# Performance work log

Measured on AMD Instinct MI355X. Metric: run time of the kernel, lower is better.

The kernel has to match this reference:

```python
import jax, jax.numpy as jnp
import numpy as np

START = 1  # strings_utils.SpecialSymbol.START
B, S, H, V = 16, 256, 512, 32000

def setup_inputs() -> dict:
    key = jax.random.key(0)
    ks = jax.random.split(key, 8)
    sc = 1.0 / np.sqrt(H)
    return {
        "target": jax.random.randint(ks[0], (B, S), 0, V, dtype=jnp.int64),
        "hidden_state": jax.random.normal(ks[1], (1, B, H), jnp.float32),
        "cell_state": jax.random.normal(ks[2], (1, B, H), jnp.float32),
        "embedding": jax.random.normal(ks[3], (V, H), jnp.float32) * 0.02,  # tied with out.weight
        "W_ih": jax.random.uniform(ks[4], (4 * H, H), jnp.float32, -sc, sc),
        "W_hh": jax.random.uniform(ks[5], (4 * H, H), jnp.float32, -sc, sc),
        "b_ih": jax.random.uniform(ks[6], (4 * H,), jnp.float32, -sc, sc),
        "b_hh": jax.random.uniform(ks[7], (4 * H,), jnp.float32, -sc, sc),
        "out_bias": jnp.zeros((V,), jnp.float32),
    }

def reference(target, hidden_state, cell_state, embedding, W_ih, W_hh, b_ih, b_hh, out_bias):
    # Teacher-forced decode: input at step 0 is START, then target[:, :-1]
    tokens = jnp.concatenate(
        [jnp.full((target.shape[0], 1), START, dtype=target.dtype), target[:, :-1]], axis=1
    )  # [B, S]
    emb = embedding[tokens]  # [B, S, H]
    # Precompute input contribution to gates for all steps (one big GEMM)
    xW = jnp.einsum("bsh,gh->bsg", emb, W_ih) + b_ih + b_hh  # [B, S, 4H]
    h0, c0 = hidden_state[0], cell_state[0]  # num_layers == 1

    def step(carry, x_t):
        h, c = carry
        gates = x_t + h @ W_hh.T  # [B, 4H]
        i, f, g, o = jnp.split(gates, 4, axis=-1)  # torch gate order: i, f, g, o
        i, f, o = jax.nn.sigmoid(i), jax.nn.sigmoid(f), jax.nn.sigmoid(o)
        g = jnp.tanh(g)
        c = f * c + i * g
        h = o * jnp.tanh(c)
        return (h, c), h

    (_, _), hs = jax.lax.scan(step, (h0, c0), jnp.swapaxes(xW, 0, 1))  # hs: [S, B, H]
    hs = jnp.swapaxes(hs, 0, 1)  # [B, S, H]
    logits = jnp.einsum("bsh,vh->bsv", hs, embedding) + out_bias  # tied projection [B, S, V]
    return logits
```

## Files before the change

kernel.cpp:

```cpp
#include <hip/hip_runtime.h>
#include <stdint.h>

#define B_N 16
#define S_N 256
#define H_N 512
#define V_N 32000
#define G4_N 2048
#define START_TOK 1
#define NBLK 16

typedef float f32x4 __attribute__((ext_vector_type(4)));
typedef int   i32x4 __attribute__((ext_vector_type(4)));
typedef unsigned short u16;
typedef u16 u16x4 __attribute__((ext_vector_type(4)));

static __device__ __forceinline__ u16 f2bf(float f) {
  unsigned u = __float_as_uint(f);
  return (u16)((u + 0x7fffu + ((u >> 16) & 1u)) >> 16);
}
static __device__ __forceinline__ float bf2f(u16 b) {
  return __uint_as_float(((unsigned)b) << 16);
}

static __device__ __forceinline__ void mfma_av(f32x4& d, i32x4 a, i32x4 b) {
  asm("v_mfma_f32_16x16x32_bf16 %0, %1, %2, %0" : "+v"(d) : "a"(a), "v"(b));
}
static __device__ __forceinline__ void mfma_vv(f32x4& d, i32x4 a, i32x4 b) {
  asm("v_mfma_f32_16x16x32_bf16 %0, %1, %2, %0" : "+v"(d) : "v"(a), "v"(b));
}

static __device__ __forceinline__ void async16(const void* g, void* l) {
  __builtin_amdgcn_global_load_lds((const __attribute__((address_space(1))) unsigned*)g,
                                   (__attribute__((address_space(3))) unsigned*)l,
                                   16, 0, 0);
}

static __device__ __forceinline__ i32x4 llc16(const void* p) {
  i32x4 v;
  asm volatile("global_load_dwordx4 %0, %1, off sc0 sc1"
               : "=v"(v) : "v"(p) : "memory");
  return v;
}

static __device__ __forceinline__ float vexp2(float x) {
  float r; asm("v_exp_f32 %0, %1\n\ts_nop 1" : "=v"(r) : "v"(x)); return r;
}
static __device__ __forceinline__ float vrcp(float x) {
  float r; asm("v_rcp_f32 %0, %1\n\ts_nop 1" : "=v"(r) : "v"(x)); return r;
}
static __device__ __forceinline__ float fsig(float x) {
  return vrcp(1.f + vexp2(-1.44269504f * x));
}
static __device__ __forceinline__ float ftanh(float x) {
  return 1.f - 2.f * vrcp(1.f + vexp2(2.88539008f * x));
}


__global__ void cast_bf16_kernel(const float* __restrict__ in, u16* __restrict__ out, int n4) {
  int i = blockIdx.x * blockDim.x + threadIdx.x;
  int stride = gridDim.x * blockDim.x;
  for (int q = i; q < n4; q += stride) {
    f32x4 v = *(const f32x4*)(in + 4l * q);
    u16x4 o;
    o.x = f2bf(v.x); o.y = f2bf(v.y); o.z = f2bf(v.z); o.w = f2bf(v.w);
    *(u16x4*)(out + 4l * q) = o;
  }
}

__global__ void init_scan_kernel(const float* __restrict__ h0, unsigned* __restrict__ Phi,
                                 unsigned* __restrict__ Plo, unsigned* __restrict__ ctr) {
  int i = blockIdx.x * blockDim.x + threadIdx.x;
  if (i < 256) ctr[i] = 0u;
  float f0 = h0[2 * i];
  float f1 = h0[2 * i + 1];
  u16 h0a = f2bf(f0), h1a = f2bf(f1);
  u16 l0a = f2bf(f0 - bf2f(h0a)), l1a = f2bf(f1 - bf2f(h1a));
  Phi[i] = (unsigned)h0a | ((unsigned)h1a << 16);
  Plo[i] = (unsigned)l0a | ((unsigned)l1a << 16);
}


__global__ __launch_bounds__(256)
void gemm_bf16_gather(const u16* __restrict__ A, const u16* __restrict__ Bm,
                      float* __restrict__ C,
                      const float* __restrict__ bias0, const float* __restrict__ bias1,
                      const int* __restrict__ target) {
  constexpr int K = H_N;
  __shared__ u16 Alds[128 * 32];
  __shared__ u16 Blds[128 * 32];
  const int tid  = threadIdx.x;
  const int lane = tid & 63;
  const int wq   = tid >> 6;
  const int mbase = blockIdx.y * 128;
  const int nbase = blockIdx.x * 128;

  const int r     = tid >> 2;
  const int off16 = (tid & 3) << 4;

  long arow0, arow1;
  {
    int m0 = mbase + r, m1 = mbase + 64 + r;
    int t0 = m0 & (S_N - 1), b0 = m0 >> 8;
    int t1 = m1 & (S_N - 1), b1 = m1 >> 8;
    arow0 = (t0 == 0) ? START_TOK : target[b0 * S_N + t0 - 1];
    arow1 = (t1 == 0) ? START_TOK : target[b1 * S_N + t1 - 1];
  }
  const long brow0 = nbase + r, brow1 = nbase + 64 + r;

  char* AldsB = (char*)Alds;
  char* BldsB = (char*)Blds;
  const char* Ab = (const char*)A;
  const char* Bb = (const char*)Bm;
  const int ldsw = wq << 10;

  const int wm   = (wq >> 1) << 6;
  const int wn   = (wq & 1) << 6;
  const int lrow = lane & 15;
  const int lk   = (lane >> 4) << 3;

  f32x4 acc[4][4] = {};

  for (int kt = 0; kt < K / 32; ++kt) {
    __syncthreads();
    const long kb = kt * 64 + off16;
    async16(Ab + arow0 * (K * 2) + kb, AldsB + ldsw);
    async16(Ab + arow1 * (K * 2) + kb, AldsB + 4096 + ldsw);
    async16(Bb + brow0 * (K * 2) + kb, BldsB + ldsw);
    async16(Bb + brow1 * (K * 2) + kb, BldsB + 4096 + ldsw);
    __syncthreads();

    i32x4 a[4], b[4];
    #pragma unroll
    for (int mi = 0; mi < 4; ++mi)
      a[mi] = *(const i32x4*)(AldsB + (((wm + mi * 16 + lrow) << 5) + lk) * 2);
    #pragma unroll
    for (int ni = 0; ni < 4; ++ni)
      b[ni] = *(const i32x4*)(BldsB + (((wn + ni * 16 + lrow) << 5) + lk) * 2);
    #pragma unroll
    for (int mi = 0; mi < 4; ++mi)
      #pragma unroll
      for (int ni = 0; ni < 4; ++ni)
        mfma_vv(acc[mi][ni], a[mi], b[ni]);
  }
  asm volatile("s_nop 7\n\ts_nop 7");

  const int rbase = (lane >> 4) << 2;
  #pragma unroll
  for (int ni = 0; ni < 4; ++ni) {
    const int col = nbase + wn + ni * 16 + lrow;
    float bv = bias0[col] + bias1[col];
    #pragma unroll
    for (int mi = 0; mi < 4; ++mi) {
      const int row = mbase + wm + mi * 16 + rbase;
      f32x4 v = acc[mi][ni];
      int b  = row >> 8, s0 = row & (S_N - 1);
      int ug = col & 511, g = col >> 9;
      size_t base = (((size_t)s0 * 64 + (ug >> 3)) * 16 + b) * 32 + (ug & 7) * 4 + g;
      C[base]         = v.x + bv;
      C[base + 32768] = v.y + bv;
      C[base + 65536] = v.z + bv;
      C[base + 98304] = v.w + bv;
    }
  }
}


__global__ __launch_bounds__(256, 1)
void gemm_bf16_logits(const u16* __restrict__ A, const u16* __restrict__ Bm,
                      float* __restrict__ C, const float* __restrict__ bias0) {
  constexpr int K = H_N;
  constexpr int N = V_N;
  __shared__ u16 Alds[128 * 32];
  __shared__ u16 Blds[256 * 32];
  const int tid  = threadIdx.x;
  const int lane = tid & 63;
  const int wq   = tid >> 6;
  const int mbase = blockIdx.y * 128;
  const int nbase = blockIdx.x * 256;

  const int r     = tid >> 2;
  const int off16 = (tid & 3) << 4;

  const long arow0 = mbase + r, arow1 = mbase + 64 + r;

  char* AldsB = (char*)Alds;
  char* BldsB = (char*)Blds;
  const char* Ab = (const char*)A;
  const char* Bb = (const char*)Bm;
  const int ldsw = wq << 10;

  const int wm   = (wq >> 1) << 6;
  const int wn   = (wq & 1) << 7;
  const int lrow = lane & 15;
  const int lk   = (lane >> 4) << 3;

  f32x4 acc[4][8] = {};

  for (int kt = 0; kt < K / 32; ++kt) {
    __syncthreads();
    const long kb = kt * 64 + off16;
    async16(Ab + arow0 * (K * 2) + kb, AldsB + ldsw);
    async16(Ab + arow1 * (K * 2) + kb, AldsB + 4096 + ldsw);
    #pragma unroll
    for (int q = 0; q < 4; ++q)
      async16(Bb + (long)(nbase + q * 64 + r) * (K * 2) + kb,
              BldsB + q * 4096 + ldsw);
    __syncthreads();

    i32x4 a[4], b[8];
    #pragma unroll
    for (int mi = 0; mi < 4; ++mi)
      a[mi] = *(const i32x4*)(AldsB + (((wm + mi * 16 + lrow) << 5) + lk) * 2);
    #pragma unroll
    for (int ni = 0; ni < 8; ++ni)
      b[ni] = *(const i32x4*)(BldsB + (((wn + ni * 16 + lrow) << 5) + lk) * 2);
    #pragma unroll
    for (int mi = 0; mi < 4; ++mi)
      #pragma unroll
      for (int ni = 0; ni < 8; ++ni)
        mfma_vv(acc[mi][ni], a[mi], b[ni]);
  }
  asm volatile("s_nop 7\n\ts_nop 7");

  const int rbase = (lane >> 4) << 2;
  #pragma unroll
  for (int ni = 0; ni < 8; ++ni) {
    const int col = nbase + wn + ni * 16 + lrow;
    float bv = bias0[col];
    #pragma unroll
    for (int mi = 0; mi < 4; ++mi) {
      const int row = mbase + wm + mi * 16 + rbase;
      f32x4 v = acc[mi][ni];
      C[(long)(row + 0) * N + col] = v.x + bv;
      C[(long)(row + 1) * N + col] = v.y + bv;
      C[(long)(row + 2) * N + col] = v.z + bv;
      C[(long)(row + 3) * N + col] = v.w + bv;
    }
  }
}


__global__ __launch_bounds__(256, 1)
void lstm_scan_coop(const float* __restrict__ xWt, const u16* __restrict__ Whh16,
                    const float* __restrict__ c0, unsigned* __restrict__ Phi,
                    unsigned* __restrict__ Plo, unsigned* __restrict__ ctr,
                    unsigned* __restrict__ hs32) {
  __shared__ __align__(16) u16 hl_hi[B_N * H_N];
  __shared__ __align__(16) u16 hl_lo[B_N * H_N];

  const int blk  = blockIdx.x;
  const int tid  = threadIdx.x;
  const int lane = tid & 63;
  const int wv   = tid >> 6;
  const int wid  = blk * 4 + wv;
  const int fr   = lane & 15;
  const int ksub = lane >> 4;
  const int b    = fr;
  char* hiB = (char*)hl_hi;
  char* loB = (char*)hl_lo;

  i32x4 afr[2][16];
  {
    const char* Wb = (const char*)Whh16;
    #pragma unroll
    for (int t = 0; t < 2; ++t) {
      long grow = (long)(fr & 3) * H_N + wid * 8 + t * 4 + (fr >> 2);
      const char* rowp = Wb + grow * (H_N * 2) + ksub * 16;
      #pragma unroll
      for (int kt = 0; kt < 16; ++kt)
        afr[t][kt] = *(const i32x4*)(rowp + kt * 64);
    }
  }

  const int ua = wid * 8 + ksub;
  const int ub = ua + 4;
  float ca = c0[b * H_N + ua];
  float cb = c0[b * H_N + ub];

  const bool stlane = ((ksub & 1) == 0);
  const int  pua    = wid * 4 + (ksub >> 1);

  {
    i32x4 th[4], tl[4];
    #pragma unroll
    for (int q = 0; q < 4; ++q) {
      int cidx = (q * 256 + tid) * 4;
      th[q] = llc16(Phi + cidx);
      tl[q] = llc16(Plo + cidx);
    }
    asm volatile("s_waitcnt vmcnt(0)" ::: "memory");
    __builtin_amdgcn_sched_barrier(0);
    #pragma unroll
    for (int q = 0; q < 4; ++q) {
      int cidx = (q * 256 + tid) * 4;
      int bb = cidx >> 8, j = cidx & 255;
      unsigned wa = (unsigned)(bb * 1024 + j * 4) ^ ((unsigned)(bb & 7) << 4);
      *(i32x4*)(hiB + wa) = th[q];
      *(i32x4*)(loB + wa) = tl[q];
    }
  }
  __syncthreads();

  const unsigned hbase = (unsigned)(fr * 1024);
  const unsigned hswz  = ((unsigned)(fr & 7)) << 4;
  const unsigned k16   = ((unsigned)ksub) << 4;

  for (int s = 0; s < S_N; ++s) {
    const float* xp = xWt + ((size_t)s * 64 + wid) * 512 + b * 32;
    f32x4 xwa = *(const f32x4*)(xp + ksub * 4);
    f32x4 xwb = *(const f32x4*)(xp + 16 + ksub * 4);

    f32x4 a00 = {0.f,0.f,0.f,0.f}, a01 = {0.f,0.f,0.f,0.f};
    f32x4 a10 = {0.f,0.f,0.f,0.f}, a11 = {0.f,0.f,0.f,0.f};
    #pragma unroll
    for (int kt = 0; kt < 16; ++kt) {
      unsigned off = (hbase + (unsigned)(kt * 64) + k16) ^ hswz;
      i32x4 bhi = *(const i32x4*)(hiB + off);
      i32x4 blo = *(const i32x4*)(loB + off);
      mfma_av(a00, afr[0][kt], bhi);
      mfma_av(a10, afr[1][kt], bhi);
      mfma_av(a01, afr[0][kt], blo);
      mfma_av(a11, afr[1][kt], blo);
    }
    asm volatile("s_nop 7\n\ts_nop 7\n\ts_nop 7");

    f32x4 ga = a00 + a01;
    f32x4 gb = a10 + a11;

    float gia = fsig(ga.x + xwa.x), gfa = fsig(ga.y + xwa.y);
    float gga = ftanh(ga.z + xwa.z), goa = fsig(ga.w + xwa.w);
    ca = gfa * ca + gia * gga;
    float ha = goa * ftanh(ca);

    float gib = fsig(gb.x + xwb.x), gfb = fsig(gb.y + xwb.y);
    float ggb = ftanh(gb.z + xwb.z), gob = fsig(gb.w + xwb.w);
    cb = gfb * cb + gib * ggb;
    float hb = gob * ftanh(cb);

    u16 ha16 = f2bf(ha), hb16 = f2bf(hb);
    u16 la16 = f2bf(ha - bf2f(ha16));
    u16 lb16 = f2bf(hb - bf2f(hb16));

    unsigned pha = (unsigned)ha16 | ((unsigned)__shfl_xor((int)(unsigned)ha16, 16) << 16);
    unsigned phb = (unsigned)hb16 | ((unsigned)__shfl_xor((int)(unsigned)hb16, 16) << 16);
    unsigned pla = (unsigned)la16 | ((unsigned)__shfl_xor((int)(unsigned)la16, 16) << 16);
    unsigned plb = (unsigned)lb16 | ((unsigned)__shfl_xor((int)(unsigned)lb16, 16) << 16);

    if (stlane) {
      hs32[((size_t)b * S_N + s) * (H_N / 2) + pua]     = pha;
      hs32[((size_t)b * S_N + s) * (H_N / 2) + pua + 2] = phb;
      if (s < S_N - 1) {
        const size_t pb = ((size_t)((s + 1) & 1) * B_N + b) * (H_N / 2);
        __hip_atomic_store(&Phi[pb + pua],     pha, __ATOMIC_RELAXED, __HIP_MEMORY_SCOPE_AGENT);
        __hip_atomic_store(&Phi[pb + pua + 2], phb, __ATOMIC_RELAXED, __HIP_MEMORY_SCOPE_AGENT);
        __hip_atomic_store(&Plo[pb + pua],     pla, __ATOMIC_RELAXED, __HIP_MEMORY_SCOPE_AGENT);
        __hip_atomic_store(&Plo[pb + pua + 2], plb, __ATOMIC_RELAXED, __HIP_MEMORY_SCOPE_AGENT);
      }
    }

    if (s == S_N - 1) break;

    __syncthreads();
    if (tid == 0) {
      __hip_atomic_fetch_add(&ctr[s], 1u, __ATOMIC_RELAXED, __HIP_MEMORY_SCOPE_AGENT);
      while (__hip_atomic_load(&ctr[s], __ATOMIC_RELAXED, __HIP_MEMORY_SCOPE_AGENT) < NBLK)
        __builtin_amdgcn_s_sleep(1);
    }
    __syncthreads();

    {
      const unsigned slotoff = (unsigned)(((s + 1) & 1) * 4096);
      i32x4 th[4], tl[4];
      #pragma unroll
      for (int q = 0; q < 4; ++q) {
        int cidx = (q * 256 + tid) * 4;
        th[q] = llc16(Phi + slotoff + cidx);
        tl[q] = llc16(Plo + slotoff + cidx);
      }
      asm volatile("s_waitcnt vmcnt(0)" ::: "memory");
      __builtin_amdgcn_sched_barrier(0);
      #pragma unroll
      for (int q = 0; q < 4; ++q) {
        int cidx = (q * 256 + tid) * 4;
        int bb = cidx >> 8, j = cidx & 255;
        unsigned wa = (unsigned)(bb * 1024 + j * 4) ^ ((unsigned)(bb & 7) << 4);
        *(i32x4*)(hiB + wa) = th[q];
        *(i32x4*)(loB + wa) = tl[q];
      }
    }
    __syncthreads();
  }
}


extern "C" void kernel_launch(void* const* d_in, const int* in_sizes, int n_in,
                              void* d_out, int out_size, void* d_ws, size_t ws_size,
                              hipStream_t stream) {
  const int*   target = (const int*)  d_in[0];
  const float* h0     = (const float*)d_in[1];
  const float* c0     = (const float*)d_in[2];
  const float* emb    = (const float*)d_in[3];
  const float* W_ih   = (const float*)d_in[4];
  const float* W_hh   = (const float*)d_in[5];
  const float* b_ih   = (const float*)d_in[6];
  const float* b_hh   = (const float*)d_in[7];
  const float* out_b  = (const float*)d_in[8];
  float* out = (float*)d_out;

  char* ws = (char*)d_ws;
  u16*      E16   = (u16*)     (ws);
  u16*      Wih16 = (u16*)     (ws + 32768000);
  u16*      Whh16 = (u16*)     (ws + 34865152);
  float*    xWt   = (float*)   (ws + 36962304);
  u16*      hs16  = (u16*)     (ws + 70516736);
  unsigned* Phi   = (unsigned*)(ws + 74711040);
  unsigned* Plo   = (unsigned*)(ws + 74743808);
  unsigned* ctr   = (unsigned*)(ws + 74776576);
  (void)ws_size; (void)in_sizes; (void)n_in; (void)out_size;

  cast_bf16_kernel<<<2048, 256, 0, stream>>>(emb,  E16,   (V_N * H_N) / 4);
  cast_bf16_kernel<<<1024, 256, 0, stream>>>(W_ih, Wih16, (G4_N * H_N) / 4);
  cast_bf16_kernel<<<1024, 256, 0, stream>>>(W_hh, Whh16, (G4_N * H_N) / 4);
  init_scan_kernel<<<16, 256, 0, stream>>>(h0, Phi, Plo, ctr);

  gemm_bf16_gather<<<dim3(G4_N / 128, (B_N * S_N) / 128), 256, 0, stream>>>(
      E16, Wih16, xWt, b_ih, b_hh, target);

  lstm_scan_coop<<<NBLK, 256, 0, stream>>>(xWt, Whh16, c0, Phi, Plo, ctr,
                                           (unsigned*)hs16);

  gemm_bf16_logits<<<dim3(V_N / 256, (B_N * S_N) / 128), 256, 0, stream>>>(
      hs16, E16, out, out_b);
}
```

Measured before the change: 1.225 ms.

## Split LSTM batch into two independent halves to overlap grid barrier latency

The recurrent scan now processes the 16 batch rows as two independent groups of 8, each with its own h exchange buffers, LDS planes and barrier counters. Phases alternate, so while one group waits on its cross-block barrier the other group's signal has already been issued, hiding barrier and global round-trip latency. Each phase still issues the full MFMA work with half the lanes' results discarded. This doubles the number of barriers and MFMA passes per step in exchange for latency overlap.

```diff
diff --git a/kernel.cpp b/kernel.cpp
--- a/kernel.cpp
+++ b/kernel.cpp
@@ -8,6 +8,8 @@
 #define G4_N 2048
 #define START_TOK 1
 #define NBLK 16
+#define HRG 8
+#define PLANE_U32 2048
 
 typedef float f32x4 __attribute__((ext_vector_type(4)));
 typedef int   i32x4 __attribute__((ext_vector_type(4)));
@@ -67,16 +69,22 @@
   }
 }
 
-__global__ void init_scan_kernel(const float* __restrict__ h0, unsigned* __restrict__ Phi,
-                                 unsigned* __restrict__ Plo, unsigned* __restrict__ ctr) {
+__global__ void init_scan_kernel(const float* __restrict__ h0,
+                                 unsigned* __restrict__ PAhi, unsigned* __restrict__ PAlo,
+                                 unsigned* __restrict__ PBhi, unsigned* __restrict__ PBlo,
+                                 unsigned* __restrict__ ctr) {
   int i = blockIdx.x * blockDim.x + threadIdx.x;
-  if (i < 256) ctr[i] = 0u;
-  float f0 = h0[2 * i];
-  float f1 = h0[2 * i + 1];
+  if (i < 512) ctr[i] = 0u;
+  int b = i >> 8, j = i & 255;
+  float f0 = h0[b * H_N + 2 * j];
+  float f1 = h0[b * H_N + 2 * j + 1];
   u16 h0a = f2bf(f0), h1a = f2bf(f1);
   u16 l0a = f2bf(f0 - bf2f(h0a)), l1a = f2bf(f1 - bf2f(h1a));
-  Phi[i] = (unsigned)h0a | ((unsigned)h1a << 16);
-  Plo[i] = (unsigned)l0a | ((unsigned)l1a << 16);
+  unsigned hw = (unsigned)h0a | ((unsigned)h1a << 16);
+  unsigned lw = (unsigned)l0a | ((unsigned)l1a << 16);
+  int idx = (b & 7) * 256 + j;
+  if (b < HRG) { PAhi[idx] = hw; PAlo[idx] = lw; }
+  else         { PBhi[idx] = hw; PBlo[idx] = lw; }
 }
 
 
@@ -240,13 +248,121 @@
 }
 
 
+static __device__ __forceinline__ void scan_phase(
+    int s, int tid, int wid, int fr, int frb, int ksub, int bAct,
+    const i32x4 (&afr)[2][16],
+    const float* __restrict__ xWt,
+    unsigned* __restrict__ Phi, unsigned* __restrict__ Plo,
+    unsigned* __restrict__ ctr,
+    char* hiB, char* loB,
+    unsigned* __restrict__ hs32,
+    float& ca, float& cb)
+{
+  const float* xp = xWt + ((size_t)s * 64 + wid) * 512 + bAct * 32;
+  f32x4 xwa = *(const f32x4*)(xp + ksub * 4);
+  f32x4 xwb = *(const f32x4*)(xp + 16 + ksub * 4);
+
+  if (s > 0) {
+    if (tid == 0) {
+      while (__hip_atomic_load(&ctr[s - 1], __ATOMIC_RELAXED,
+                               __HIP_MEMORY_SCOPE_AGENT) < NBLK)
+        __builtin_amdgcn_s_sleep(1);
+    }
+    __syncthreads();
+  }
+
+  {
+    const unsigned slotoff = (unsigned)((s & 1) * PLANE_U32);
+    i32x4 th[2], tl[2];
+    #pragma unroll
+    for (int q = 0; q < 2; ++q) {
+      int cidx = (q * 256 + tid) * 4;
+      th[q] = llc16(Phi + slotoff + cidx);
+      tl[q] = llc16(Plo + slotoff + cidx);
+    }
+    asm volatile("s_waitcnt vmcnt(0)" ::: "memory");
+    __builtin_amdgcn_sched_barrier(0);
+    #pragma unroll
+    for (int q = 0; q < 2; ++q) {
+      int cidx = (q * 256 + tid) * 4;
+      int row = cidx >> 8, j = cidx & 255;
+      unsigned wa = (unsigned)(row * 1024 + j * 4) ^ ((unsigned)row << 4);
+      *(i32x4*)(hiB + wa) = th[q];
+      *(i32x4*)(loB + wa) = tl[q];
+    }
+  }
+  __syncthreads();
+
+  const unsigned hbase = (unsigned)(frb * 1024);
+  const unsigned hswz  = (unsigned)frb << 4;
+  const unsigned k16   = (unsigned)ksub << 4;
+  f32x4 a00 = {0.f,0.f,0.f,0.f}, a01 = {0.f,0.f,0.f,0.f};
+  f32x4 a10 = {0.f,0.f,0.f,0.f}, a11 = {0.f,0.f,0.f,0.f};
+  #pragma unroll
+  for (int kt = 0; kt < 16; ++kt) {
+    unsigned off = (hbase + (unsigned)(kt * 64) + k16) ^ hswz;
+    i32x4 bhi = *(const i32x4*)(hiB + off);
+    i32x4 blo = *(const i32x4*)(loB + off);
+    mfma_av(a00, afr[0][kt], bhi);
+    mfma_av(a10, afr[1][kt], bhi);
+    mfma_av(a01, afr[0][kt], blo);
+    mfma_av(a11, afr[1][kt], blo);
+  }
+  asm volatile("s_nop 7\n\ts_nop 7\n\ts_nop 7");
+
+  f32x4 ga = a00 + a01;
+  f32x4 gb = a10 + a11;
+
+  float gia = fsig(ga.x + xwa.x), gfa = fsig(ga.y + xwa.y);
+  float gga = ftanh(ga.z + xwa.z), goa = fsig(ga.w + xwa.w);
+  ca = gfa * ca + gia * gga;
+  float ha = goa * ftanh(ca);
+
+  float gib = fsig(gb.x + xwb.x), gfb = fsig(gb.y + xwb.y);
+  float ggb = ftanh(gb.z + xwb.z), gob = fsig(gb.w + xwb.w);
+  cb = gfb * cb + gib * ggb;
+  float hb = gob * ftanh(cb);
+
+  u16 ha16 = f2bf(ha), hb16 = f2bf(hb);
+  u16 la16 = f2bf(ha - bf2f(ha16));
+  u16 lb16 = f2bf(hb - bf2f(hb16));
+
+  unsigned pha = (unsigned)ha16 | ((unsigned)__shfl_xor((int)(unsigned)ha16, 16) << 16);
+  unsigned phb = (unsigned)hb16 | ((unsigned)__shfl_xor((int)(unsigned)hb16, 16) << 16);
+  unsigned pla = (unsigned)la16 | ((unsigned)__shfl_xor((int)(unsigned)la16, 16) << 16);
+  unsigned plb = (unsigned)lb16 | ((unsigned)__shfl_xor((int)(unsigned)lb16, 16) << 16);
+
+  const int pua = wid * 4 + (ksub >> 1);
+  if (((ksub & 1) == 0) && fr < HRG) {
+    hs32[((size_t)bAct * S_N + s) * (H_N / 2) + pua]     = pha;
+    hs32[((size_t)bAct * S_N + s) * (H_N / 2) + pua + 2] = phb;
+    if (s < S_N - 1) {
+      const size_t pb = (size_t)(((s + 1) & 1) * PLANE_U32) + (size_t)frb * 256;
+      __hip_atomic_store(&Phi[pb + pua],     pha, __ATOMIC_RELAXED, __HIP_MEMORY_SCOPE_AGENT);
+      __hip_atomic_store(&Phi[pb + pua + 2], phb, __ATOMIC_RELAXED, __HIP_MEMORY_SCOPE_AGENT);
+      __hip_atomic_store(&Plo[pb + pua],     pla, __ATOMIC_RELAXED, __HIP_MEMORY_SCOPE_AGENT);
+      __hip_atomic_store(&Plo[pb + pua + 2], plb, __ATOMIC_RELAXED, __HIP_MEMORY_SCOPE_AGENT);
+    }
+  }
+
+  if (s < S_N - 1) {
+    __syncthreads();
+    if (tid == 0)
+      __hip_atomic_fetch_add(&ctr[s], 1u, __ATOMIC_RELAXED, __HIP_MEMORY_SCOPE_AGENT);
+  }
+}
+
 __global__ __launch_bounds__(256, 1)
 void lstm_scan_coop(const float* __restrict__ xWt, const u16* __restrict__ Whh16,
-                    const float* __restrict__ c0, unsigned* __restrict__ Phi,
-                    unsigned* __restrict__ Plo, unsigned* __restrict__ ctr,
+                    const float* __restrict__ c0,
+                    unsigned* __restrict__ PAhi, unsigned* __restrict__ PAlo,
+                    unsigned* __restrict__ PBhi, unsigned* __restrict__ PBlo,
+                    unsigned* __restrict__ ctr,
                     unsigned* __restrict__ hs32) {
-  __shared__ __align__(16) u16 hl_hi[B_N * H_N];
-  __shared__ __align__(16) u16 hl_lo[B_N * H_N];
+  __shared__ __align__(16) u16 lAhi[HRG * H_N];
+  __shared__ __align__(16) u16 lAlo[HRG * H_N];
+  __shared__ __align__(16) u16 lBhi[HRG * H_N];
+  __shared__ __align__(16) u16 lBlo[HRG * H_N];
 
   const int blk  = blockIdx.x;
   const int tid  = threadIdx.x;
@@ -254,10 +370,10 @@
   const int wv   = tid >> 6;
   const int wid  = blk * 4 + wv;
   const int fr   = lane & 15;
+  const int frb  = fr & 7;
   const int ksub = lane >> 4;
-  const int b    = fr;
-  char* hiB = (char*)hl_hi;
-  char* loB = (char*)hl_lo;
+  const int bA   = frb;
+  const int bB   = frb + HRG;
 
   i32x4 afr[2][16];
   {
@@ -274,121 +390,14 @@
 
   const int ua = wid * 8 + ksub;
   const int ub = ua + 4;
-  float ca = c0[b * H_N + ua];
-  float cb = c0[b * H_N + ub];
-
-  const bool stlane = ((ksub & 1) == 0);
-  const int  pua    = wid * 4 + (ksub >> 1);
-
-  {
-    i32x4 th[4], tl[4];
-    #pragma unroll
-    for (int q = 0; q < 4; ++q) {
-      int cidx = (q * 256 + tid) * 4;
-      th[q] = llc16(Phi + cidx);
-      tl[q] = llc16(Plo + cidx);
-    }
-    asm volatile("s_waitcnt vmcnt(0)" ::: "memory");
-    __builtin_amdgcn_sched_barrier(0);
-    #pragma unroll
-    for (int q = 0; q < 4; ++q) {
-      int cidx = (q * 256 + tid) * 4;
-      int bb = cidx >> 8, j = cidx & 255;
-      unsigned wa = (unsigned)(bb * 1024 + j * 4) ^ ((unsigned)(bb & 7) << 4);
-      *(i32x4*)(hiB + wa) = th[q];
-      *(i32x4*)(loB + wa) = tl[q];
-    }
-  }
-  __syncthreads();
-
-  const unsigned hbase = (unsigned)(fr * 1024);
-  const unsigned hswz  = ((unsigned)(fr & 7)) << 4;
-  const unsigned k16   = ((unsigned)ksub) << 4;
+  float caA = c0[bA * H_N + ua], cbA = c0[bA * H_N + ub];
+  float caB = c0[bB * H_N + ua], cbB = c0[bB * H_N + ub];
 
   for (int s = 0; s < S_N; ++s) {
-    const float* xp = xWt + ((size_t)s * 64 + wid) * 512 + b * 32;
-    f32x4 xwa = *(const f32x4*)(xp + ksub * 4);
-    f32x4 xwb = *(const f32x4*)(xp + 16 + ksub * 4);
-
-    f32x4 a00 = {0.f,0.f,0.f,0.f}, a01 = {0.f,0.f,0.f,0.f};
-    f32x4 a10 = {0.f,0.f,0.f,0.f}, a11 = {0.f,0.f,0.f,0.f};
-    #pragma unroll
-    for (int kt = 0; kt < 16; ++kt) {
-      unsigned off = (hbase + (unsigned)(kt * 64) + k16) ^ hswz;
-      i32x4 bhi = *(const i32x4*)(hiB + off);
-      i32x4 blo = *(const i32x4*)(loB + off);
-      mfma_av(a00, afr[0][kt], bhi);
-      mfma_av(a10, afr[1][kt], bhi);
-      mfma_av(a01, afr[0][kt], blo);
-      mfma_av(a11, afr[1][kt], blo);
-    }
-    asm volatile("s_nop 7\n\ts_nop 7\n\ts_nop 7");
-
-    f32x4 ga = a00 + a01;
-    f32x4 gb = a10 + a11;
-
-    float gia = fsig(ga.x + xwa.x), gfa = fsig(ga.y + xwa.y);
-    float gga = ftanh(ga.z + xwa.z), goa = fsig(ga.w + xwa.w);
-    ca = gfa * ca + gia * gga;
-    float ha = goa * ftanh(ca);
-
-    float gib = fsig(gb.x + xwb.x), gfb = fsig(gb.y + xwb.y);
-    float ggb = ftanh(gb.z + xwb.z), gob = fsig(gb.w + xwb.w);
-    cb = gfb * cb + gib * ggb;
-    float hb = gob * ftanh(cb);
-
-    u16 ha16 = f2bf(ha), hb16 = f2bf(hb);
-    u16 la16 = f2bf(ha - bf2f(ha16));
-    u16 lb16 = f2bf(hb - bf2f(hb16));
-
-    unsigned pha = (unsigned)ha16 | ((unsigned)__shfl_xor((int)(unsigned)ha16, 16) << 16);
-    unsigned phb = (unsigned)hb16 | ((unsigned)__shfl_xor((int)(unsigned)hb16, 16) << 16);
-    unsigned pla = (unsigned)la16 | ((unsigned)__shfl_xor((int)(unsigned)la16, 16) << 16);
-    unsigned plb = (unsigned)lb16 | ((unsigned)__shfl_xor((int)(unsigned)lb16, 16) << 16);
-
-    if (stlane) {
-      hs32[((size_t)b * S_N + s) * (H_N / 2) + pua]     = pha;
-      hs32[((size_t)b * S_N + s) * (H_N / 2) + pua + 2] = phb;
-      if (s < S_N - 1) {
-        const size_t pb = ((size_t)((s + 1) & 1) * B_N + b) * (H_N / 2);
-        __hip_atomic_store(&Phi[pb + pua],     pha, __ATOMIC_RELAXED, __HIP_MEMORY_SCOPE_AGENT);
-        __hip_atomic_store(&Phi[pb + pua + 2], phb, __ATOMIC_RELAXED, __HIP_MEMORY_SCOPE_AGENT);
-        __hip_atomic_store(&Plo[pb + pua],     pla, __ATOMIC_RELAXED, __HIP_MEMORY_SCOPE_AGENT);
-        __hip_atomic_store(&Plo[pb + pua + 2], plb, __ATOMIC_RELAXED, __HIP_MEMORY_SCOPE_AGENT);
-      }
-    }
-
-    if (s == S_N - 1) break;
-
-    __syncthreads();
-    if (tid == 0) {
-      __hip_atomic_fetch_add(&ctr[s], 1u, __ATOMIC_RELAXED, __HIP_MEMORY_SCOPE_AGENT);
-      while (__hip_atomic_load(&ctr[s], __ATOMIC_RELAXED, __HIP_MEMORY_SCOPE_AGENT) < NBLK)
-        __builtin_amdgcn_s_sleep(1);
-    }
-    __syncthreads();
-
-    {
-      const unsigned slotoff = (unsigned)(((s + 1) & 1) * 4096);
-      i32x4 th[4], tl[4];
-      #pragma unroll
-      for (int q = 0; q < 4; ++q) {
-        int cidx = (q * 256 + tid) * 4;
-        th[q] = llc16(Phi + slotoff + cidx);
-        tl[q] = llc16(Plo + slotoff + cidx);
-      }
-      asm volatile("s_waitcnt vmcnt(0)" ::: "memory");
-      __builtin_amdgcn_sched_barrier(0);
-      #pragma unroll
-      for (int q = 0; q < 4; ++q) {
-        int cidx = (q * 256 + tid) * 4;
-        int bb = cidx >> 8, j = cidx & 255;
-        unsigned wa = (unsigned)(bb * 1024 + j * 4) ^ ((unsigned)(bb & 7) << 4);
-        *(i32x4*)(hiB + wa) = th[q];
-        *(i32x4*)(loB + wa) = tl[q];
-      }
-    }
-    __syncthreads();
+    scan_phase(s, tid, wid, fr, frb, ksub, bA, afr, xWt, PAhi, PAlo, ctr,
+               (char*)lAhi, (char*)lAlo, hs32, caA, cbA);
+    scan_phase(s, tid, wid, fr, frb, ksub, bB, afr, xWt, PBhi, PBlo, ctr + 256,
+               (char*)lBhi, (char*)lBlo, hs32, caB, cbB);
   }
 }
 
@@ -413,21 +422,23 @@
   u16*      Whh16 = (u16*)     (ws + 34865152);
   float*    xWt   = (float*)   (ws + 36962304);
   u16*      hs16  = (u16*)     (ws + 70516736);
-  unsigned* Phi   = (unsigned*)(ws + 74711040);
-  unsigned* Plo   = (unsigned*)(ws + 74743808);
+  unsigned* PAhi  = (unsigned*)(ws + 74711040);
+  unsigned* PAlo  = (unsigned*)(ws + 74727424);
+  unsigned* PBhi  = (unsigned*)(ws + 74743808);
+  unsigned* PBlo  = (unsigned*)(ws + 74760192);
   unsigned* ctr   = (unsigned*)(ws + 74776576);
   (void)ws_size; (void)in_sizes; (void)n_in; (void)out_size;
 
   cast_bf16_kernel<<<2048, 256, 0, stream>>>(emb,  E16,   (V_N * H_N) / 4);
   cast_bf16_kernel<<<1024, 256, 0, stream>>>(W_ih, Wih16, (G4_N * H_N) / 4);
   cast_bf16_kernel<<<1024, 256, 0, stream>>>(W_hh, Whh16, (G4_N * H_N) / 4);
-  init_scan_kernel<<<16, 256, 0, stream>>>(h0, Phi, Plo, ctr);
+  init_scan_kernel<<<16, 256, 0, stream>>>(h0, PAhi, PAlo, PBhi, PBlo, ctr);
 
   gemm_bf16_gather<<<dim3(G4_N / 128, (B_N * S_N) / 128), 256, 0, stream>>>(
       E16, Wih16, xWt, b_ih, b_hh, target);
 
-  lstm_scan_coop<<<NBLK, 256, 0, stream>>>(xWt, Whh16, c0, Phi, Plo, ctr,
-                                           (unsigned*)hs16);
+  lstm_scan_coop<<<NBLK, 256, 0, stream>>>(xWt, Whh16, c0, PAhi, PAlo,
+                                           PBhi, PBlo, ctr, (unsigned*)hs16);
 
   gemm_bf16_logits<<<dim3(V_N / 256, (B_N * S_N) / 128), 256, 0, stream>>>(
       hs16, E16, out, out_b);
```

New measurement: 1.570 ms. 1.28x slower.
